# Optimization experiments

Hardware: AMD Instinct MI355X
Metric: run time of the kernel (lower is better)

The kernel has to match this reference:

```python
import jax, jax.numpy as jnp
import numpy as np

S, C, H, D = 4096, 2048, 16, 128  # seq, channels, heads, head_dim
EPS = 1.1920929e-07  # torch F.rms_norm default eps = finfo(float32).eps


def setup_inputs() -> dict:
    key = jax.random.key(0)
    ks = jax.random.split(key, 12)
    w = 0.02
    return {
        "x": jax.random.normal(ks[0], (S, C), dtype=jnp.float32),
        "rope": jax.random.normal(ks[1], (S, 1, D // 2, 2, 2), dtype=jnp.float32),
        "Wq": jax.random.normal(ks[2], (C, C), dtype=jnp.float32) * w,
        "bq": jnp.zeros((C,), dtype=jnp.float32),
        "Wk": jax.random.normal(ks[3], (C, C), dtype=jnp.float32) * w,
        "bk": jnp.zeros((C,), dtype=jnp.float32),
        "Wv": jax.random.normal(ks[4], (C, C), dtype=jnp.float32) * w,
        "bv": jnp.zeros((C,), dtype=jnp.float32),
        "qn_w": jnp.ones((D,), dtype=jnp.float32),
        "kn_w": jnp.ones((D,), dtype=jnp.float32),
        "Wo": jax.random.normal(ks[5], (C, C), dtype=jnp.float32) * w,
        "bo": jnp.zeros((C,), dtype=jnp.float32),
    }


def _rms_norm(x, weight):
    # RMSNorm over last dim, as F.rms_norm
    inv = jax.lax.rsqrt(jnp.mean(x * x, axis=-1, keepdims=True) + EPS)
    return x * inv * weight


def _apply_rotary(x, rope):
    # x: [S, H, D]; rope: [S, 1, D//2, 2, 2]
    s, h, d = x.shape
    x_ = x.reshape(s, h, d // 2, 1, 2)
    out = (rope * x_).sum(axis=-1)  # [S, H, D//2, 2]
    return out.reshape(s, h, d)


def reference(x, rope, Wq, bq, Wk, bk, Wv, bv, qn_w, kn_w, Wo, bo):
    # QKV projections -> [S, H, D]
    q = (x @ Wq.T + bq).reshape(S, H, D)
    k = (x @ Wk.T + bk).reshape(S, H, D)
    v = (x @ Wv.T + bv).reshape(S, H, D)
    # RMSNorm on q/k per head_dim
    q = _rms_norm(q, qn_w)
    k = _rms_norm(k, kn_w)
    # Custom rotary (table-driven 2x2 rotation)
    q = _apply_rotary(q, rope)
    k = _apply_rotary(k, rope)
    # Dense scaled dot-product attention over seq, per head
    scale = 1.0 / jnp.sqrt(jnp.asarray(D, dtype=q.dtype))
    scores = jnp.einsum("shd,thd->hst", q, k) * scale  # [H, S, S]
    probs = jax.nn.softmax(scores, axis=-1)
    out = jnp.einsum("hst,thd->shd", probs, v).reshape(S, C)
    return out @ Wo.T + bo
```

## Files before the change

kernel.cpp:

```cpp
#include <hip/hip_runtime.h>

#define S 4096
#define C 2048
#define H 16
#define D 128
#define EPS 1.1920929e-07f
#define QSCALE (0.08838834764831845f * 1.4426950408889634f)

typedef __attribute__((ext_vector_type(8))) short short8;
typedef __attribute__((ext_vector_type(4))) float f32x4;
typedef __attribute__((ext_vector_type(4))) unsigned short ushort4v;

#if __has_builtin(__builtin_amdgcn_mfma_f32_16x16x16bf16_1k)
#define HAVE_MFMA16 1
#else
#define HAVE_MFMA16 0
#endif

#if __has_builtin(__builtin_amdgcn_exp2f)
#define EXP2F __builtin_amdgcn_exp2f
#else
#define EXP2F exp2f
#endif

__device__ __forceinline__ unsigned short f2bf(float f) {
  unsigned int u = __builtin_bit_cast(unsigned int, f);
  u += 0x7fff + ((u >> 16) & 1);
  return (unsigned short)(u >> 16);
}
__device__ __forceinline__ float bf2f(unsigned short v) {
  unsigned int u = ((unsigned int)v) << 16;
  return __builtin_bit_cast(float, u);
}
__device__ __forceinline__ unsigned int pkbf(float a, float b) {
  return (unsigned int)f2bf(a) | ((unsigned int)f2bf(b) << 16);
}
__device__ __forceinline__ unsigned int pkbf_trunc(float a, float b) {
  return __builtin_amdgcn_perm(__builtin_bit_cast(unsigned int, b),
                               __builtin_bit_cast(unsigned int, a), 0x07060302);
}
__device__ __forceinline__ float lo16f(unsigned int d) {
  return __builtin_bit_cast(float, d << 16);
}
__device__ __forceinline__ float hi16f(unsigned int d) {
  return __builtin_bit_cast(float, d & 0xffff0000u);
}
__device__ __forceinline__ void gld16(const unsigned short* g, unsigned short* l) {
  __builtin_amdgcn_global_load_lds(
      (const __attribute__((address_space(1))) unsigned int*)g,
      (__attribute__((address_space(3))) unsigned int*)l, 16, 0, 0);
}

__global__ void cvt_kernel(const float* __restrict__ src,
                           unsigned short* __restrict__ dst, int n) {
  int i = (blockIdx.x * 256 + threadIdx.x) * 4;
  if (i >= n) return;
  float4 v = *(const float4*)(src + i);
  ushort4 o;
  o.x = f2bf(v.x); o.y = f2bf(v.y); o.z = f2bf(v.z); o.w = f2bf(v.w);
  *(ushort4*)(dst + i) = o;
}
__global__ void cvtw_kernel(const float* __restrict__ w0, const float* __restrict__ w1,
                            const float* __restrict__ w2, const float* __restrict__ w3,
                            unsigned short* __restrict__ dst) {
  const float* srcs[4] = {w0, w1, w2, w3};
  const float* src = srcs[blockIdx.y];
  int i = (blockIdx.x * 256 + threadIdx.x) * 4;
  float4 v = *(const float4*)(src + i);
  ushort4 o;
  o.x = f2bf(v.x); o.y = f2bf(v.y); o.z = f2bf(v.z); o.w = f2bf(v.w);
  *(ushort4*)(dst + (size_t)blockIdx.y * C * C + i) = o;
}
__global__ void bias_concat(const float* __restrict__ bq, const float* __restrict__ bk,
                            const float* __restrict__ bv, float* __restrict__ dst) {
  int i = blockIdx.x * 256 + threadIdx.x;
  const float* s = (i < C) ? bq : ((i < 2 * C) ? bk : bv);
  dst[i] = s[i & (C - 1)];
}

__global__ __launch_bounds__(256) void gemm_bt(const unsigned short* __restrict__ A,
                                               const unsigned short* __restrict__ B,
                                               const float* __restrict__ bias,
                                               float* __restrict__ outf,
                                               unsigned short* __restrict__ qh,
                                               unsigned short* __restrict__ kh,
                                               unsigned short* __restrict__ vt,
                                               int N, int mode) {
  __shared__ __align__(16) unsigned short U[128 * 136];
  unsigned short* Al = U;
  unsigned short* Bl = U + 128 * 64;
  const int t = threadIdx.x, w = t >> 6, lane = t & 63;
  const int lq = lane & 15, quad = lane >> 4;
  const int wm = w & 1, wn = w >> 1;
  const int m0 = blockIdx.y * 128, n0 = blockIdx.x * 128;
  f32x4 acc[4][4] = {};
  float biasv[4];
#pragma unroll
  for (int nt = 0; nt < 4; nt++) biasv[nt] = bias[n0 + wn * 64 + nt * 16 + lq];
  const int sr = lane >> 3, sg = lane & 7;
  for (int k0 = 0; k0 < C; k0 += 64) {
    __syncthreads();
#pragma unroll
    for (int p = 0; p < 4; p++) {
      int row = w * 32 + p * 8 + sr;
      int c = sg ^ (row & 7);
      gld16(A + (size_t)(m0 + row) * C + k0 + c * 8, &Al[(w * 32 + p * 8) * 64]);
      gld16(B + (size_t)(n0 + row) * C + k0 + c * 8, &Bl[(w * 32 + p * 8) * 64]);
    }
    __syncthreads();
#pragma unroll
    for (int ks = 0; ks < 2; ks++) {
      short8 af[4], bf[4];
#pragma unroll
      for (int mt = 0; mt < 4; mt++) {
        int row = wm * 64 + mt * 16 + lq;
        af[mt] = *(const short8*)&Al[row * 64 + ((ks * 4 + quad) ^ (lq & 7)) * 8];
      }
#pragma unroll
      for (int nt = 0; nt < 4; nt++) {
        int row = wn * 64 + nt * 16 + lq;
        bf[nt] = *(const short8*)&Bl[row * 64 + ((ks * 4 + quad) ^ (lq & 7)) * 8];
      }
#pragma unroll
      for (int mt = 0; mt < 4; mt++)
#pragma unroll
        for (int nt = 0; nt < 4; nt++)
          acc[mt][nt] = __builtin_amdgcn_mfma_f32_16x16x32_bf16(af[mt], bf[nt], acc[mt][nt], 0, 0, 0);
    }
  }

  if (mode == 0) {
#pragma unroll
    for (int mt = 0; mt < 4; mt++)
#pragma unroll
      for (int nt = 0; nt < 4; nt++) {
        int n = n0 + wn * 64 + nt * 16 + lq;
#pragma unroll
        for (int r = 0; r < 4; r++) {
          int m = m0 + wm * 64 + mt * 16 + quad * 4 + r;
          outf[(size_t)m * N + n] = acc[mt][nt][r] + biasv[nt];
        }
      }
    return;
  }

  const int gh = n0 >> 7;
  __syncthreads();
  const int rr = t >> 4, ck = t & 15;
  if (gh < 32) {
#pragma unroll
    for (int mt = 0; mt < 4; mt++)
#pragma unroll
      for (int nt = 0; nt < 4; nt++) {
        int dloc = wn * 64 + nt * 16 + lq;
#pragma unroll
        for (int r = 0; r < 4; r++)
          U[(wm * 64 + mt * 16 + quad * 4 + r) * 136 + dloc] = f2bf(acc[mt][nt][r] + biasv[nt]);
      }
    __syncthreads();
    unsigned short* dst = ((gh < 16) ? qh : kh) + (size_t)(gh & 15) * S * D;
#pragma unroll
    for (int p = 0; p < 8; p++) {
      int m = p * 16 + rr;
      uint4 vv = *(const uint4*)&U[m * 136 + ck * 8];
      *(uint4*)(dst + (size_t)(m0 + m) * D + ck * 8) = vv;
    }
  } else {
#pragma unroll
    for (int mt = 0; mt < 4; mt++)
#pragma unroll
      for (int nt = 0; nt < 4; nt++) {
        int dloc = wn * 64 + nt * 16 + lq;
        int mloc = wm * 64 + mt * 16 + quad * 4;
        *(unsigned int*)&U[dloc * 136 + mloc] =
            pkbf(acc[mt][nt][0] + biasv[nt], acc[mt][nt][1] + biasv[nt]);
        *(unsigned int*)&U[dloc * 136 + mloc + 2] =
            pkbf(acc[mt][nt][2] + biasv[nt], acc[mt][nt][3] + biasv[nt]);
      }
    __syncthreads();
    unsigned short* dst = vt + (size_t)(gh - 32) * D * S;
#pragma unroll
    for (int p = 0; p < 8; p++) {
      int d = p * 16 + rr;
      uint4 vv = *(const uint4*)&U[d * 136 + ck * 8];
      *(uint4*)(dst + (size_t)d * S + m0 + ck * 8) = vv;
    }
  }
}

__global__ __launch_bounds__(256) void rmsrope_kernel(unsigned short* __restrict__ qh,
                                                      unsigned short* __restrict__ kh,
                                                      const float* __restrict__ qn_w,
                                                      const float* __restrict__ kn_w,
                                                      const float* __restrict__ rope) {
  const int which = blockIdx.y;
  unsigned short* io = which ? kh : qh;
  const float* wgt = which ? kn_w : qn_w;
  const float scale = which ? 1.0f : QSCALE;
  int wid = (blockIdx.x * 256 + threadIdx.x) >> 6;
  int lane = threadIdx.x & 63;
  int s = wid & (S - 1);
  unsigned short* row = io + (size_t)wid * D;
  unsigned int pr = *(unsigned int*)(row + lane * 2);
  float a = bf2f((unsigned short)(pr & 0xffff));
  float b = bf2f((unsigned short)(pr >> 16));
  float ss = a * a + b * b;
  for (int m = 1; m < 64; m <<= 1) ss += __shfl_xor(ss, m);
  float inv = rsqrtf(ss * (1.0f / 128.0f) + EPS) * scale;
  float2 wv = *(const float2*)(wgt + lane * 2);
  float an = a * inv * wv.x, bn = b * inv * wv.y;
  float4 r = *(const float4*)(rope + (size_t)s * 256 + lane * 4);
  *(unsigned int*)(row + lane * 2) = pkbf(r.x * an + r.y * bn, r.z * an + r.w * bn);
}

__global__ __launch_bounds__(256, 2) void flash_kernel(const unsigned short* __restrict__ qh,
                                                       const unsigned short* __restrict__ kh,
                                                       const unsigned short* __restrict__ vt,
                                                       unsigned short* __restrict__ ao) {
  __shared__ __align__(16) unsigned short Klds[128 * 128];
  __shared__ __align__(16) unsigned short Vlds[128 * 128];
  const int h = blockIdx.y, i0 = blockIdx.x * 128;
  const int t = threadIdx.x, w = t >> 6, lane = t & 63;
  const int lq = lane & 15, quad = lane >> 4;

  const unsigned short* Qbase = qh + ((size_t)h * S + i0 + w * 32 + lq) * D;
  short8 qfrag[2][4];
#pragma unroll
  for (int qi = 0; qi < 2; qi++)
#pragma unroll
    for (int kt = 0; kt < 4; kt++)
      qfrag[qi][kt] = *(const short8*)(Qbase + (size_t)qi * 16 * D + kt * 32 + quad * 8);

  f32x4 oacc[2][8] = {};
  float lrun[2] = {0.0f, 0.0f};
  const unsigned short* Kbase = kh + (size_t)h * S * D;
  const unsigned short* Vbase = vt + (size_t)h * D * S;

  const int kr = lane >> 4, kg = lane & 15;

  for (int j0 = 0; j0 < S; j0 += 128) {
    __syncthreads();
#pragma unroll
    for (int p = 0; p < 8; p++) {
      int krow = w * 32 + p * 4 + kr;
      gld16(Kbase + (size_t)(j0 + krow) * D + (kg ^ (krow & 7)) * 8,
            &Klds[(w * 32 + p * 4) * 128]);
      gld16(Vbase + (size_t)krow * S + j0 + (kg ^ (krow & 7)) * 8,
            &Vlds[(w * 32 + p * 4) * 128]);
    }
    __syncthreads();

    f32x4 sacc[2][8] = {};
#pragma unroll
    for (int kt = 0; kt < 4; kt++)
#pragma unroll
      for (int nt = 0; nt < 8; nt++) {
        int row = nt * 16 + lq;
        short8 af = *(const short8*)&Klds[row * 128 + (((kt * 4 + quad) ^ (row & 7)) * 8)];
        sacc[0][nt] = __builtin_amdgcn_mfma_f32_16x16x32_bf16(af, qfrag[0][kt], sacc[0][nt], 0, 0, 0);
        sacc[1][nt] = __builtin_amdgcn_mfma_f32_16x16x32_bf16(af, qfrag[1][kt], sacc[1][nt], 0, 0, 0);
      }

    unsigned int pd[2][8][2];
#pragma unroll
    for (int qi = 0; qi < 2; qi++) {
      float rsum = 0.0f;
#pragma unroll
      for (int nt = 0; nt < 8; nt++) {
        float e0 = EXP2F(sacc[qi][nt][0]);
        float e1 = EXP2F(sacc[qi][nt][1]);
        float e2 = EXP2F(sacc[qi][nt][2]);
        float e3 = EXP2F(sacc[qi][nt][3]);
        unsigned int d0 = pkbf_trunc(e0, e1);
        unsigned int d1 = pkbf_trunc(e2, e3);
        pd[qi][nt][0] = d0;
        pd[qi][nt][1] = d1;
        rsum += (lo16f(d0) + hi16f(d0)) + (lo16f(d1) + hi16f(d1));
      }
      lrun[qi] += rsum;
    }

#if HAVE_MFMA16
#pragma unroll
    for (int ntk = 0; ntk < 8; ntk++) {
      ushort4v a0 = __builtin_bit_cast(ushort4v, make_uint2(pd[0][ntk][0], pd[0][ntk][1]));
      ushort4v a1 = __builtin_bit_cast(ushort4v, make_uint2(pd[1][ntk][0], pd[1][ntk][1]));
      int g = 2 * ntk + (quad >> 1), go = (quad & 1) * 4;
#pragma unroll
      for (int dt = 0; dt < 8; dt++) {
        int row = dt * 16 + lq;
        ushort4v bf = *(const ushort4v*)&Vlds[row * 128 + ((g ^ (row & 7)) * 8) + go];
        oacc[0][dt] = __builtin_amdgcn_mfma_f32_16x16x16bf16_1k(a0, bf, oacc[0][dt], 0, 0, 0);
        oacc[1][dt] = __builtin_amdgcn_mfma_f32_16x16x16bf16_1k(a1, bf, oacc[1][dt], 0, 0, 0);
      }
    }
#else
    __syncthreads();
    {
      unsigned short* Pw = Klds + w * 16 * 136;
#pragma unroll
      for (int qi = 0; qi < 2; qi++) {
#pragma unroll
        for (int nt = 0; nt < 8; nt++) {
          *(unsigned int*)&Pw[lq * 136 + nt * 16 + quad * 4] = pd[qi][nt][0];
          *(unsigned int*)&Pw[lq * 136 + nt * 16 + quad * 4 + 2] = pd[qi][nt][1];
        }
#pragma unroll
        for (int kt = 0; kt < 4; kt++) {
          short8 af = *(const short8*)&Pw[lq * 136 + kt * 32 + quad * 8];
#pragma unroll
          for (int dt = 0; dt < 8; dt++) {
            int row = dt * 16 + lq;
            short8 bf = *(const short8*)&Vlds[row * 128 + (((kt * 4 + quad) ^ (row & 7)) * 8)];
            oacc[qi][dt] = __builtin_amdgcn_mfma_f32_16x16x32_bf16(af, bf, oacc[qi][dt], 0, 0, 0);
          }
        }
      }
    }
#endif
  }

#pragma unroll
  for (int qi = 0; qi < 2; qi++) {
    lrun[qi] += __shfl_xor(lrun[qi], 16);
    lrun[qi] += __shfl_xor(lrun[qi], 32);
  }
  float il[2][4];
#pragma unroll
  for (int qi = 0; qi < 2; qi++)
#pragma unroll
    for (int r = 0; r < 4; r++) il[qi][r] = 1.0f / __shfl(lrun[qi], quad * 4 + r);
#pragma unroll
  for (int qi = 0; qi < 2; qi++)
#pragma unroll
    for (int dt = 0; dt < 8; dt++)
#pragma unroll
      for (int r = 0; r < 4; r++)
        ao[(size_t)(i0 + w * 32 + qi * 16 + quad * 4 + r) * C + h * 128 + dt * 16 + lq] =
            f2bf(oacc[qi][dt][r] * il[qi][r]);
}

extern "C" void kernel_launch(void* const* d_in, const int* in_sizes, int n_in,
                              void* d_out, int out_size, void* d_ws, size_t ws_size,
                              hipStream_t stream) {
  const float* x    = (const float*)d_in[0];
  const float* rope = (const float*)d_in[1];
  const float* Wq   = (const float*)d_in[2];
  const float* bq   = (const float*)d_in[3];
  const float* Wk   = (const float*)d_in[4];
  const float* bk   = (const float*)d_in[5];
  const float* Wv   = (const float*)d_in[6];
  const float* bv   = (const float*)d_in[7];
  const float* qn_w = (const float*)d_in[8];
  const float* kn_w = (const float*)d_in[9];
  const float* Wo   = (const float*)d_in[10];
  const float* bo   = (const float*)d_in[11];
  float* out = (float*)d_out;

  unsigned short* xb  = (unsigned short*)d_ws;
  unsigned short* wqb = xb + (size_t)S * C;
  unsigned short* wob = wqb + (size_t)3 * C * C;
  unsigned short* qh  = wqb + (size_t)4 * C * C;
  unsigned short* kh  = qh + (size_t)S * C;
  unsigned short* vt  = kh + (size_t)S * C;
  unsigned short* ao  = vt + (size_t)S * C;
  float* bqkv = (float*)(ao + (size_t)S * C);

  cvt_kernel<<<S * C / 1024, 256, 0, stream>>>(x, xb, S * C);
  cvtw_kernel<<<dim3(C * C / 1024, 4), 256, 0, stream>>>(Wq, Wk, Wv, Wo, wqb);
  bias_concat<<<3 * C / 256, 256, 0, stream>>>(bq, bk, bv, bqkv);

  gemm_bt<<<dim3(3 * C / 128, S / 128), 256, 0, stream>>>(
      xb, wqb, bqkv, nullptr, qh, kh, vt, 3 * C, 1);

  rmsrope_kernel<<<dim3((H * S) / 4, 2), 256, 0, stream>>>(qh, kh, qn_w, kn_w, rope);

  flash_kernel<<<dim3(S / 128, H), 256, 0, stream>>>(qh, kh, vt, ao);

  gemm_bt<<<dim3(C / 128, S / 128), 256, 0, stream>>>(
      ao, wob, bo, out, nullptr, nullptr, nullptr, C, 0);
}
```

Before: 503.0 us.

## Permute V-transpose layout so PV uses 16x16x32 MFMA directly from registers

The V projection epilogue now writes the transposed V with a permuted sequence ordering inside each 32-wide group. The exponentiated score registers can then be packed straight into 8-element A fragments for the 16x16x32 bf16 MFMA, instead of using twice as many 16x16x16 MFMAs. Fewer, wider MFMAs and wider LDS reads for V are meant to cut issue overhead in the PV loop. It also adds s_setprio around the MFMA blocks, and relies on the permuted layout matching the register order exactly.

```diff
diff --git a/kernel.cpp b/kernel.cpp
--- a/kernel.cpp
+++ b/kernel.cpp
@@ -9,13 +9,7 @@
 
 typedef __attribute__((ext_vector_type(8))) short short8;
 typedef __attribute__((ext_vector_type(4))) float f32x4;
-typedef __attribute__((ext_vector_type(4))) unsigned short ushort4v;
-
-#if __has_builtin(__builtin_amdgcn_mfma_f32_16x16x16bf16_1k)
-#define HAVE_MFMA16 1
-#else
-#define HAVE_MFMA16 0
-#endif
+typedef __attribute__((ext_vector_type(4))) unsigned int uint4v;
 
 #if __has_builtin(__builtin_amdgcn_exp2f)
 #define EXP2F __builtin_amdgcn_exp2f
@@ -49,6 +43,12 @@
   __builtin_amdgcn_global_load_lds(
       (const __attribute__((address_space(1))) unsigned int*)g,
       (__attribute__((address_space(3))) unsigned int*)l, 16, 0, 0);
+}
+__device__ __forceinline__ short8 mk_a(unsigned int a, unsigned int b,
+                                       unsigned int c, unsigned int d) {
+  uint4v u;
+  u[0] = a; u[1] = b; u[2] = c; u[3] = d;
+  return __builtin_bit_cast(short8, u);
 }
 
 __global__ void cvt_kernel(const float* __restrict__ src,
@@ -166,15 +166,15 @@
       *(uint4*)(dst + (size_t)(m0 + m) * D + ck * 8) = vv;
     }
   } else {
-#pragma unroll
+    #pragma unroll
     for (int mt = 0; mt < 4; mt++)
 #pragma unroll
       for (int nt = 0; nt < 4; nt++) {
         int dloc = wn * 64 + nt * 16 + lq;
-        int mloc = wm * 64 + mt * 16 + quad * 4;
-        *(unsigned int*)&U[dloc * 136 + mloc] =
+        int mlocP = wm * 64 + (mt >> 1) * 32 + quad * 8 + (mt & 1) * 4;
+        *(unsigned int*)&U[dloc * 136 + mlocP] =
             pkbf(acc[mt][nt][0] + biasv[nt], acc[mt][nt][1] + biasv[nt]);
-        *(unsigned int*)&U[dloc * 136 + mloc + 2] =
+        *(unsigned int*)&U[dloc * 136 + mlocP + 2] =
             pkbf(acc[mt][nt][2] + biasv[nt], acc[mt][nt][3] + biasv[nt]);
       }
     __syncthreads();
@@ -251,6 +251,7 @@
     __syncthreads();
 
     f32x4 sacc[2][8] = {};
+    __builtin_amdgcn_s_setprio(1);
 #pragma unroll
     for (int kt = 0; kt < 4; kt++)
 #pragma unroll
@@ -260,6 +261,7 @@
         sacc[0][nt] = __builtin_amdgcn_mfma_f32_16x16x32_bf16(af, qfrag[0][kt], sacc[0][nt], 0, 0, 0);
         sacc[1][nt] = __builtin_amdgcn_mfma_f32_16x16x32_bf16(af, qfrag[1][kt], sacc[1][nt], 0, 0, 0);
       }
+    __builtin_amdgcn_s_setprio(0);
 
     unsigned int pd[2][8][2];
 #pragma unroll
@@ -280,44 +282,20 @@
       lrun[qi] += rsum;
     }
 
-#if HAVE_MFMA16
-#pragma unroll
-    for (int ntk = 0; ntk < 8; ntk++) {
-      ushort4v a0 = __builtin_bit_cast(ushort4v, make_uint2(pd[0][ntk][0], pd[0][ntk][1]));
-      ushort4v a1 = __builtin_bit_cast(ushort4v, make_uint2(pd[1][ntk][0], pd[1][ntk][1]));
-      int g = 2 * ntk + (quad >> 1), go = (quad & 1) * 4;
+    __builtin_amdgcn_s_setprio(1);
+#pragma unroll
+    for (int kk = 0; kk < 4; kk++) {
+      short8 a0 = mk_a(pd[0][2 * kk][0], pd[0][2 * kk][1], pd[0][2 * kk + 1][0], pd[0][2 * kk + 1][1]);
+      short8 a1 = mk_a(pd[1][2 * kk][0], pd[1][2 * kk][1], pd[1][2 * kk + 1][0], pd[1][2 * kk + 1][1]);
 #pragma unroll
       for (int dt = 0; dt < 8; dt++) {
         int row = dt * 16 + lq;
-        ushort4v bf = *(const ushort4v*)&Vlds[row * 128 + ((g ^ (row & 7)) * 8) + go];
-        oacc[0][dt] = __builtin_amdgcn_mfma_f32_16x16x16bf16_1k(a0, bf, oacc[0][dt], 0, 0, 0);
-        oacc[1][dt] = __builtin_amdgcn_mfma_f32_16x16x16bf16_1k(a1, bf, oacc[1][dt], 0, 0, 0);
-      }
-    }
-#else
-    __syncthreads();
-    {
-      unsigned short* Pw = Klds + w * 16 * 136;
-#pragma unroll
-      for (int qi = 0; qi < 2; qi++) {
-#pragma unroll
-        for (int nt = 0; nt < 8; nt++) {
-          *(unsigned int*)&Pw[lq * 136 + nt * 16 + quad * 4] = pd[qi][nt][0];
-          *(unsigned int*)&Pw[lq * 136 + nt * 16 + quad * 4 + 2] = pd[qi][nt][1];
-        }
-#pragma unroll
-        for (int kt = 0; kt < 4; kt++) {
-          short8 af = *(const short8*)&Pw[lq * 136 + kt * 32 + quad * 8];
-#pragma unroll
-          for (int dt = 0; dt < 8; dt++) {
-            int row = dt * 16 + lq;
-            short8 bf = *(const short8*)&Vlds[row * 128 + (((kt * 4 + quad) ^ (row & 7)) * 8)];
-            oacc[qi][dt] = __builtin_amdgcn_mfma_f32_16x16x32_bf16(af, bf, oacc[qi][dt], 0, 0, 0);
-          }
-        }
-      }
-    }
-#endif
+        short8 bf = *(const short8*)&Vlds[row * 128 + (((kk * 4 + quad) ^ (row & 7)) * 8)];
+        oacc[0][dt] = __builtin_amdgcn_mfma_f32_16x16x32_bf16(a0, bf, oacc[0][dt], 0, 0, 0);
+        oacc[1][dt] = __builtin_amdgcn_mfma_f32_16x16x32_bf16(a1, bf, oacc[1][dt], 0, 0, 0);
+      }
+    }
+    __builtin_amdgcn_s_setprio(0);
   }
 
 #pragma unroll
```

Measured after the change: 472.0 us. 6.2% less time.
